# Kernel optimization log

Hardware: AMD Instinct MI355X
Metric: run time of the kernel (lower is better)

## Reference

```python
import jax, jax.numpy as jnp
import numpy as np

RES = 128
B = 16


def setup_inputs() -> dict:
    key = jax.random.key(0)
    k_space_input = jax.random.normal(key, (B, 1, RES, RES, 2), dtype=jnp.float32)
    # full-grid init trajectory: every (i, j) shifted by -res/2, shape [res^2, 2]
    ii, jj = jnp.meshgrid(jnp.arange(RES), jnp.arange(RES), indexing='ij')
    trajectory = (jnp.stack([ii, jj], axis=-1).reshape(-1, 2).astype(jnp.float32)
                  - 0.5 * RES)
    return {"k_space_input": k_space_input, "trajectory": trajectory}


def _bilinear_sample(img, traj):
    # img: [B, 2, H, W] real k-space channels; traj: [M, 2] in [-H/2, H/2)
    Bn, C, H, W = img.shape
    pr = traj[:, 0] + 0.5 * H  # continuous row coords [M]
    pc = traj[:, 1] + 0.5 * W  # continuous col coords [M]
    r0f = jnp.floor(pr)
    c0f = jnp.floor(pc)
    wr = pr - r0f  # differentiable fractional weights
    wc = pc - c0f
    r0 = jnp.clip(r0f.astype(jnp.int32), 0, H - 1)
    r1 = jnp.clip(r0 + 1, 0, H - 1)
    c0 = jnp.clip(c0f.astype(jnp.int32), 0, W - 1)
    c1 = jnp.clip(c0 + 1, 0, W - 1)
    g = lambda r, c: img[:, :, r, c]  # gather -> [B, C, M]
    sub = ((1 - wr) * (1 - wc) * g(r0, c0)
           + (1 - wr) * wc * g(r0, c1)
           + wr * (1 - wc) * g(r1, c0)
           + wr * wc * g(r1, c1))
    return sub  # [B, 2, M]


def reference(k_space_input, trajectory):
    # permute(0,1,4,2,3).squeeze(1): [B,1,H,W,2] -> [B,2,H,W]
    x = jnp.transpose(k_space_input, (0, 1, 4, 2, 3))[:, 0]
    Bn, C, H, W = x.shape
    # learned-trajectory bilinear interpolation of k-space (grid_sample analogue)
    sub = _bilinear_sample(x, trajectory)            # [B, 2, M]
    s = sub[:, 0] + 1j * sub[:, 1]                   # [B, M] complex64
    # adjoint NUFFT (type-1 direct DFT), separable over the two axes
    xs = (jnp.arange(H) - H // 2).astype(jnp.float32)
    ys = (jnp.arange(W) - W // 2).astype(jnp.float32)
    two_pi = np.float32(2.0 * np.pi)
    Ex = jnp.exp(1j * (two_pi / H) * trajectory[:, 0:1] * xs[None, :])  # [M, H]
    Ey = jnp.exp(1j * (two_pi / W) * trajectory[:, 1:2] * ys[None, :])  # [M, W]
    tmp = s[:, :, None] * Ey[None, :, :]             # [B, M, W] complex64
    out = jnp.einsum('mh,bmw->bhw', Ex, tmp)         # [B, H, W] complex64
    out2 = jnp.stack([out.real, out.imag], axis=1)   # [B, 2, H, W]
    return out2[:, None]                             # unsqueeze(1) -> [B, 1, 2, H, W]
```

## Files before the change

### kernel.cpp

```cpp
#include <hip/hip_runtime.h>

#define RES 128
#define NB 16
#define NPTS (RES * RES)


__device__ __forceinline__ void cmac(float2& a, float2 u, float2 v) {
    a.x = fmaf(u.x, v.x, fmaf(-u.y, v.y, a.x));
    a.y = fmaf(u.x, v.y, fmaf( u.y, v.x, a.y));
}

__global__ __launch_bounds__(512) void kB_colpass(
    const float* __restrict__ kin, const float* __restrict__ traj,
    float2* __restrict__ T)
{
    __shared__ float2 sS[8][RES];
    __shared__ float2 FyT[32][RES];
    const float TWO_PI = 6.283185307179586f;
    const int b  = blockIdx.x >> 4;
    const int i0 = (blockIdx.x & 15) * 8;
    const int tid = threadIdx.x;

    const float2* img = (const float2*)kin;
    #pragma unroll
    for (int k = 0; k < 2; ++k) {
        int idx = tid + k * 512;
        int ii = idx >> 7;
        int j  = idx & (RES - 1);
        int m  = (i0 + ii) * RES + j;
        float pr = traj[2 * m + 0] + 0.5f * RES;
        float pc = traj[2 * m + 1] + 0.5f * RES;
        float r0f = floorf(pr), c0f = floorf(pc);
        float wr = pr - r0f, wc = pc - c0f;
        int r0 = min(max((int)r0f, 0), RES - 1);
        int r1 = min(r0 + 1, RES - 1);
        int c0 = min(max((int)c0f, 0), RES - 1);
        int c1 = min(c0 + 1, RES - 1);
        const float2* pb = img + b * NPTS;
        float2 g00 = pb[r0 * RES + c0], g01 = pb[r0 * RES + c1];
        float2 g10 = pb[r1 * RES + c0], g11 = pb[r1 * RES + c1];
        float w00 = (1.f - wr) * (1.f - wc), w01 = (1.f - wr) * wc;
        float w10 = wr * (1.f - wc),         w11 = wr * wc;
        sS[ii][j] = make_float2(
            w00 * g00.x + w01 * g01.x + w10 * g10.x + w11 * g11.x,
            w00 * g00.y + w01 * g01.y + w10 * g10.y + w11 * g11.y);
    }
    __syncthreads();

    const int w = tid & (RES - 1);
    const int g = tid >> 7;
    float2 a0 = make_float2(0.f, 0.f), a1 = make_float2(0.f, 0.f);

    const int jl = tid >> 4;
    const int w0 = (tid & 15) * 8;

    for (int jt = 0; jt < 4; ++jt) {
        float bj = traj[2 * (32 * jt + jl) + 1];
        float th = (TWO_PI / RES) * bj;
        float sn0, cs0, snr, csr;
        sincosf(th * (float)(w0 - RES / 2), &sn0, &cs0);
        sincosf(th, &snr, &csr);
        float zx = cs0, zy = sn0;
        #pragma unroll
        for (int k = 0; k < 8; ++k) {
            FyT[jl][w0 + k] = make_float2(zx, zy);
            float nx = fmaf(zx, csr, -zy * snr);
            zy = fmaf(zx, snr, zy * csr);
            zx = nx;
        }
        __syncthreads();

        #pragma unroll 8
        for (int jj = 0; jj < 32; ++jj) {
            float2 fy = FyT[jj][w];
            float2 s0 = sS[2 * g + 0][32 * jt + jj];
            float2 s1 = sS[2 * g + 1][32 * jt + jj];
            cmac(a0, s0, fy);
            cmac(a1, s1, fy);
        }
        __syncthreads();
    }

    T[(b * RES + i0 + 2 * g + 0) * RES + w] = a0;
    T[(b * RES + i0 + 2 * g + 1) * RES + w] = a1;
}

__global__ __launch_bounds__(512) void kC_rowpass(
    const float2* __restrict__ T, const float* __restrict__ traj,
    float* __restrict__ out)
{
    __shared__ float2 fS[8][RES];
    const float TWO_PI = 6.283185307179586f;
    const int b  = blockIdx.x >> 4;
    const int h0 = (blockIdx.x & 15) * 8;
    const int tid = threadIdx.x;

    #pragma unroll
    for (int k = 0; k < 2; ++k) {
        int idx = tid + k * 512;
        int hh = idx >> 7;
        int i  = idx & (RES - 1);
        float ai = traj[2 * (i * RES) + 0];
        float ang = (TWO_PI / RES) * ai * (float)(h0 + hh - RES / 2);
        float sn, cs;
        sincosf(ang, &sn, &cs);
        fS[hh][i] = make_float2(cs, sn);
    }
    __syncthreads();

    const int w = tid & (RES - 1);
    const int g = tid >> 7;
    float2 a0 = make_float2(0.f, 0.f), a1 = make_float2(0.f, 0.f);

    #pragma unroll 4
    for (int i = 0; i < RES; ++i) {
        float2 t = T[(b * RES + i) * RES + w];
        float2 f0 = fS[2 * g + 0][i];
        float2 f1 = fS[2 * g + 1][i];
        cmac(a0, f0, t);
        cmac(a1, f1, t);
    }

    int h = h0 + 2 * g;
    out[((b * 2 + 0) * RES + h) * RES + w] = a0.x;
    out[((b * 2 + 1) * RES + h) * RES + w] = a0.y;
    out[((b * 2 + 0) * RES + h + 1) * RES + w] = a1.x;
    out[((b * 2 + 1) * RES + h + 1) * RES + w] = a1.y;
}

extern "C" void kernel_launch(void* const* d_in, const int* in_sizes, int n_in,
                              void* d_out, int out_size, void* d_ws, size_t ws_size,
                              hipStream_t stream) {
    const float* kin  = (const float*)d_in[0];
    const float* traj = (const float*)d_in[1];
    float* out = (float*)d_out;

    float2* T = (float2*)d_ws;

    kB_colpass<<<NB * (RES / 8), 512, 0, stream>>>(kin, traj, T);
    kC_rowpass<<<NB * (RES / 8), 512, 0, stream>>>(T, traj, out);
}
```

Baseline: 29.77 us.

## Fuse column and row passes into one cooperative kernel with grid sync

Merges the two NUFFT pass kernels into a single cooperative launch that writes the intermediate T, issues a threadfence and grid-wide sync, then runs the row pass in the same blocks. Shared memory from the first pass is reused for the row-pass twiddles. The aim is to remove the second kernel launch and its inter-kernel gap. It adds grid-sync overhead and requires all 256 blocks of 512 threads to be co-resident.

```diff
diff --git a/kernel.cpp b/kernel.cpp
--- a/kernel.cpp
+++ b/kernel.cpp
@@ -1,4 +1,7 @@
 #include <hip/hip_runtime.h>
+#include <hip/hip_cooperative_groups.h>
+
+namespace cg = cooperative_groups;
 
 #define RES 128
 #define NB 16
@@ -10,16 +13,18 @@
     a.y = fmaf(u.x, v.y, fmaf( u.y, v.x, a.y));
 }
 
-__global__ __launch_bounds__(512) void kB_colpass(
+__global__ __launch_bounds__(512) void fused_nufft(
     const float* __restrict__ kin, const float* __restrict__ traj,
-    float2* __restrict__ T)
+    float2* __restrict__ T, float* __restrict__ out)
 {
     __shared__ float2 sS[8][RES];
     __shared__ float2 FyT[32][RES];
     const float TWO_PI = 6.283185307179586f;
     const int b  = blockIdx.x >> 4;
-    const int i0 = (blockIdx.x & 15) * 8;
+    const int t8 = (blockIdx.x & 15) * 8;
     const int tid = threadIdx.x;
+    const int w = tid & (RES - 1);
+    const int g = tid >> 7;
 
     const float2* img = (const float2*)kin;
     #pragma unroll
@@ -27,7 +32,7 @@
         int idx = tid + k * 512;
         int ii = idx >> 7;
         int j  = idx & (RES - 1);
-        int m  = (i0 + ii) * RES + j;
+        int m  = (t8 + ii) * RES + j;
         float pr = traj[2 * m + 0] + 0.5f * RES;
         float pc = traj[2 * m + 1] + 0.5f * RES;
         float r0f = floorf(pr), c0f = floorf(pc);
@@ -47,10 +52,7 @@
     }
     __syncthreads();
 
-    const int w = tid & (RES - 1);
-    const int g = tid >> 7;
     float2 a0 = make_float2(0.f, 0.f), a1 = make_float2(0.f, 0.f);
-
     const int jl = tid >> 4;
     const int w0 = (tid & 15) * 8;
 
@@ -81,19 +83,11 @@
         __syncthreads();
     }
 
-    T[(b * RES + i0 + 2 * g + 0) * RES + w] = a0;
-    T[(b * RES + i0 + 2 * g + 1) * RES + w] = a1;
-}
+    T[(b * RES + t8 + 2 * g + 0) * RES + w] = a0;
+    T[(b * RES + t8 + 2 * g + 1) * RES + w] = a1;
 
-__global__ __launch_bounds__(512) void kC_rowpass(
-    const float2* __restrict__ T, const float* __restrict__ traj,
-    float* __restrict__ out)
-{
-    __shared__ float2 fS[8][RES];
-    const float TWO_PI = 6.283185307179586f;
-    const int b  = blockIdx.x >> 4;
-    const int h0 = (blockIdx.x & 15) * 8;
-    const int tid = threadIdx.x;
+    __threadfence();
+    cg::this_grid().sync();
 
     #pragma unroll
     for (int k = 0; k < 2; ++k) {
@@ -101,31 +95,28 @@
         int hh = idx >> 7;
         int i  = idx & (RES - 1);
         float ai = traj[2 * (i * RES) + 0];
-        float ang = (TWO_PI / RES) * ai * (float)(h0 + hh - RES / 2);
+        float ang = (TWO_PI / RES) * ai * (float)(t8 + hh - RES / 2);
         float sn, cs;
         sincosf(ang, &sn, &cs);
-        fS[hh][i] = make_float2(cs, sn);
+        sS[hh][i] = make_float2(cs, sn);
     }
     __syncthreads();
 
-    const int w = tid & (RES - 1);
-    const int g = tid >> 7;
-    float2 a0 = make_float2(0.f, 0.f), a1 = make_float2(0.f, 0.f);
-
+    float2 b0 = make_float2(0.f, 0.f), b1 = make_float2(0.f, 0.f);
     #pragma unroll 4
     for (int i = 0; i < RES; ++i) {
-        float2 t = T[(b * RES + i) * RES + w];
-        float2 f0 = fS[2 * g + 0][i];
-        float2 f1 = fS[2 * g + 1][i];
-        cmac(a0, f0, t);
-        cmac(a1, f1, t);
+        float2 tv = T[(b * RES + i) * RES + w];
+        float2 f0 = sS[2 * g + 0][i];
+        float2 f1 = sS[2 * g + 1][i];
+        cmac(b0, f0, tv);
+        cmac(b1, f1, tv);
     }
 
-    int h = h0 + 2 * g;
-    out[((b * 2 + 0) * RES + h) * RES + w] = a0.x;
-    out[((b * 2 + 1) * RES + h) * RES + w] = a0.y;
-    out[((b * 2 + 0) * RES + h + 1) * RES + w] = a1.x;
-    out[((b * 2 + 1) * RES + h + 1) * RES + w] = a1.y;
+    int h = t8 + 2 * g;
+    out[((b * 2 + 0) * RES + h) * RES + w] = b0.x;
+    out[((b * 2 + 1) * RES + h) * RES + w] = b0.y;
+    out[((b * 2 + 0) * RES + h + 1) * RES + w] = b1.x;
+    out[((b * 2 + 1) * RES + h + 1) * RES + w] = b1.y;
 }
 
 extern "C" void kernel_launch(void* const* d_in, const int* in_sizes, int n_in,
@@ -134,9 +125,9 @@
     const float* kin  = (const float*)d_in[0];
     const float* traj = (const float*)d_in[1];
     float* out = (float*)d_out;
-
     float2* T = (float2*)d_ws;
 
-    kB_colpass<<<NB * (RES / 8), 512, 0, stream>>>(kin, traj, T);
-    kC_rowpass<<<NB * (RES / 8), 512, 0, stream>>>(T, traj, out);
+    void* args[] = {(void*)&kin, (void*)&traj, (void*)&T, (void*)&out};
+    hipLaunchCooperativeKernel((void*)fused_nufft, dim3(NB * (RES / 8)), dim3(512),
+                               args, 0, stream);
 }
```

Result: slower. 105.9 us (+255.9%).

## Halve block size, use hardware sin/cos in revolutions, cache trajectory column in LDS

Applied to the files above, without the earlier changes.

Both passes now launch twice as many 256-thread blocks, each covering 4 rows instead of 8, which doubles the grid on a GPU with many CUs. The twiddle factors now come from the native AMDGCN sin/cos builtins on fractional revolutions instead of sincosf plus a rotation recurrence, removing range-reduction cost. The col-pass caches the trajectory column coordinates in LDS and reorganises its barriers. The trade-offs are more blocks each recomputing the twiddle table and some loss of accuracy from the hardware trig approximations.

```diff
diff --git a/kernel.cpp b/kernel.cpp
--- a/kernel.cpp
+++ b/kernel.cpp
@@ -4,69 +4,66 @@
 #define NB 16
 #define NPTS (RES * RES)
 
-
 __device__ __forceinline__ void cmac(float2& a, float2 u, float2 v) {
     a.x = fmaf(u.x, v.x, fmaf(-u.y, v.y, a.x));
     a.y = fmaf(u.x, v.y, fmaf( u.y, v.x, a.y));
 }
 
-__global__ __launch_bounds__(512) void kB_colpass(
+__device__ __forceinline__ float2 cis_rev(float rev) {
+    float r = __builtin_amdgcn_fractf(rev);
+    return make_float2(__builtin_amdgcn_cosf(r), __builtin_amdgcn_sinf(r));
+}
+
+__global__ __launch_bounds__(256) void kB_colpass(
     const float* __restrict__ kin, const float* __restrict__ traj,
     float2* __restrict__ T)
 {
-    __shared__ float2 sS[8][RES];
+    __shared__ float2 sS[4][RES];
     __shared__ float2 FyT[32][RES];
-    const float TWO_PI = 6.283185307179586f;
-    const int b  = blockIdx.x >> 4;
-    const int i0 = (blockIdx.x & 15) * 8;
+    __shared__ float  bjS[RES];
+    const int b   = blockIdx.x >> 5;
+    const int i0  = (blockIdx.x & 31) * 4;
     const int tid = threadIdx.x;
+    const int w   = tid & (RES - 1);
+    const int g   = tid >> 7;
 
-    const float2* img = (const float2*)kin;
+    const float2* img = (const float2*)kin + b * NPTS;
+    const float2* tp  = (const float2*)traj;
+
+    if (tid < RES) bjS[tid] = tp[tid].y;
+
     #pragma unroll
     for (int k = 0; k < 2; ++k) {
-        int idx = tid + k * 512;
+        int idx = tid + k * 256;
         int ii = idx >> 7;
         int j  = idx & (RES - 1);
-        int m  = (i0 + ii) * RES + j;
-        float pr = traj[2 * m + 0] + 0.5f * RES;
-        float pc = traj[2 * m + 1] + 0.5f * RES;
+        float2 t2 = tp[(i0 + ii) * RES + j];
+        float pr = t2.x + 64.f, pc = t2.y + 64.f;
         float r0f = floorf(pr), c0f = floorf(pc);
         float wr = pr - r0f, wc = pc - c0f;
         int r0 = min(max((int)r0f, 0), RES - 1);
         int r1 = min(r0 + 1, RES - 1);
         int c0 = min(max((int)c0f, 0), RES - 1);
         int c1 = min(c0 + 1, RES - 1);
-        const float2* pb = img + b * NPTS;
-        float2 g00 = pb[r0 * RES + c0], g01 = pb[r0 * RES + c1];
-        float2 g10 = pb[r1 * RES + c0], g11 = pb[r1 * RES + c1];
+        float2 g00 = img[r0 * RES + c0], g01 = img[r0 * RES + c1];
+        float2 g10 = img[r1 * RES + c0], g11 = img[r1 * RES + c1];
         float w00 = (1.f - wr) * (1.f - wc), w01 = (1.f - wr) * wc;
         float w10 = wr * (1.f - wc),         w11 = wr * wc;
         sS[ii][j] = make_float2(
             w00 * g00.x + w01 * g01.x + w10 * g10.x + w11 * g11.x,
             w00 * g00.y + w01 * g01.y + w10 * g10.y + w11 * g11.y);
     }
-    __syncthreads();
 
-    const int w = tid & (RES - 1);
-    const int g = tid >> 7;
     float2 a0 = make_float2(0.f, 0.f), a1 = make_float2(0.f, 0.f);
-
-    const int jl = tid >> 4;
-    const int w0 = (tid & 15) * 8;
+    const float wf = (float)(w - 64) * 0.0078125f;
+    const int jh = 16 * g;
 
     for (int jt = 0; jt < 4; ++jt) {
-        float bj = traj[2 * (32 * jt + jl) + 1];
-        float th = (TWO_PI / RES) * bj;
-        float sn0, cs0, snr, csr;
-        sincosf(th * (float)(w0 - RES / 2), &sn0, &cs0);
-        sincosf(th, &snr, &csr);
-        float zx = cs0, zy = sn0;
+        __syncthreads();
         #pragma unroll
-        for (int k = 0; k < 8; ++k) {
-            FyT[jl][w0 + k] = make_float2(zx, zy);
-            float nx = fmaf(zx, csr, -zy * snr);
-            zy = fmaf(zx, snr, zy * csr);
-            zx = nx;
+        for (int jj = 0; jj < 16; ++jj) {
+            float bj = bjS[32 * jt + jh + jj];
+            FyT[jh + jj][w] = cis_rev(bj * wf);
         }
         __syncthreads();
 
@@ -78,54 +75,52 @@
             cmac(a0, s0, fy);
             cmac(a1, s1, fy);
         }
-        __syncthreads();
     }
 
     T[(b * RES + i0 + 2 * g + 0) * RES + w] = a0;
     T[(b * RES + i0 + 2 * g + 1) * RES + w] = a1;
 }
 
-__global__ __launch_bounds__(512) void kC_rowpass(
+__global__ __launch_bounds__(256) void kC_rowpass(
     const float2* __restrict__ T, const float* __restrict__ traj,
     float* __restrict__ out)
 {
-    __shared__ float2 fS[8][RES];
-    const float TWO_PI = 6.283185307179586f;
-    const int b  = blockIdx.x >> 4;
-    const int h0 = (blockIdx.x & 15) * 8;
+    __shared__ float2 fS[4][RES];
+    const int b   = blockIdx.x >> 5;
+    const int h0  = (blockIdx.x & 31) * 4;
     const int tid = threadIdx.x;
+    const int w   = tid & (RES - 1);
+    const int g   = tid >> 7;
+
+    const float2* tp = (const float2*)traj;
 
     #pragma unroll
     for (int k = 0; k < 2; ++k) {
-        int idx = tid + k * 512;
+        int idx = tid + k * 256;
         int hh = idx >> 7;
         int i  = idx & (RES - 1);
-        float ai = traj[2 * (i * RES) + 0];
-        float ang = (TWO_PI / RES) * ai * (float)(h0 + hh - RES / 2);
-        float sn, cs;
-        sincosf(ang, &sn, &cs);
-        fS[hh][i] = make_float2(cs, sn);
+        float ai = tp[i * RES].x;
+        fS[hh][i] = cis_rev(ai * (float)(h0 + hh - 64) * 0.0078125f);
     }
     __syncthreads();
 
-    const int w = tid & (RES - 1);
-    const int g = tid >> 7;
-    float2 a0 = make_float2(0.f, 0.f), a1 = make_float2(0.f, 0.f);
-
-    #pragma unroll 4
+    const float2* Tb = T + b * NPTS;
+    float2 b0 = make_float2(0.f, 0.f), b1 = make_float2(0.f, 0.f);
+    #pragma unroll 8
     for (int i = 0; i < RES; ++i) {
-        float2 t = T[(b * RES + i) * RES + w];
+        float2 tv = Tb[i * RES + w];
         float2 f0 = fS[2 * g + 0][i];
         float2 f1 = fS[2 * g + 1][i];
-        cmac(a0, f0, t);
-        cmac(a1, f1, t);
+        cmac(b0, f0, tv);
+        cmac(b1, f1, tv);
     }
 
+    float* o = out + b * 2 * NPTS;
     int h = h0 + 2 * g;
-    out[((b * 2 + 0) * RES + h) * RES + w] = a0.x;
-    out[((b * 2 + 1) * RES + h) * RES + w] = a0.y;
-    out[((b * 2 + 0) * RES + h + 1) * RES + w] = a1.x;
-    out[((b * 2 + 1) * RES + h + 1) * RES + w] = a1.y;
+    o[h * RES + w]              = b0.x;
+    o[NPTS + h * RES + w]       = b0.y;
+    o[(h + 1) * RES + w]        = b1.x;
+    o[NPTS + (h + 1) * RES + w] = b1.y;
 }
 
 extern "C" void kernel_launch(void* const* d_in, const int* in_sizes, int n_in,
@@ -134,9 +129,8 @@
     const float* kin  = (const float*)d_in[0];
     const float* traj = (const float*)d_in[1];
     float* out = (float*)d_out;
-
     float2* T = (float2*)d_ws;
 
-    kB_colpass<<<NB * (RES / 8), 512, 0, stream>>>(kin, traj, T);
-    kC_rowpass<<<NB * (RES / 8), 512, 0, stream>>>(T, traj, out);
+    kB_colpass<<<NB * (RES / 4), 256, 0, stream>>>(kin, traj, T);
+    kC_rowpass<<<NB * (RES / 4), 256, 0, stream>>>(T, traj, out);
 }
```

Result: faster. 26.07 us (-12.4%).
